# Performance work log

Measured on AMD Instinct MI355X. Metric: run time of the kernel, lower is better.

## Reference

```python
import jax, jax.numpy as jnp
import numpy as np

NUM_CODES = 8192
DIM = 512
COMMITMENT_COST = 0.25


def setup_inputs() -> dict:
    key = jax.random.key(0)
    kx, kc = jax.random.split(key)
    x = jax.random.normal(kx, (8, 4096, DIM), dtype=jnp.float32)
    # nn.init.uniform_(codebook.weight, -1/num_codes, 1/num_codes)
    bound = 1.0 / NUM_CODES
    codebook = jax.random.uniform(kc, (NUM_CODES, DIM), dtype=jnp.float32,
                                  minval=-bound, maxval=bound)
    return {"x": x, "codebook": codebook}


def reference(x, codebook):
    orig_shape = x.shape
    flat = x.reshape(-1, orig_shape[-1])              # [N, D]
    # Squared-distance expansion (argmin-equivalent to torch.cdist's L2):
    # ||f||^2 - 2 f.c + ||c||^2
    x_sq = jnp.sum(flat * flat, axis=-1, keepdims=True)          # [N, 1]
    c_sq = jnp.sum(codebook * codebook, axis=-1)                 # [K]
    dists = x_sq - 2.0 * jnp.einsum('nd,kd->nk', flat, codebook) + c_sq  # [N, K]
    indices_flat = jnp.argmin(dists, axis=-1)                    # [N] int
    quantized_flat = codebook[indices_flat]                      # [N, D]
    # codebook_loss = mse(quantized, sg(flat)); commitment = mse(flat, sg(quantized))
    codebook_loss = jnp.mean((quantized_flat - jax.lax.stop_gradient(flat)) ** 2)
    commitment_loss = jnp.mean((flat - jax.lax.stop_gradient(quantized_flat)) ** 2)
    vq_loss = codebook_loss + COMMITMENT_COST * commitment_loss
    # straight-through
    quantized_st = flat + jax.lax.stop_gradient(quantized_flat - flat)
    return (quantized_st.reshape(orig_shape), vq_loss,
            indices_flat.reshape(orig_shape[:-1]))
```

## Files before the change

### kernel.cpp

```cpp
#include <hip/hip_runtime.h>


#define NROWS 32768
#define KCODES 8192
#define DD 512
#define CAP 24
#define MARGIN 2.5e-4f

typedef __bf16 bf16_t;
typedef __bf16 bf16x4 __attribute__((ext_vector_type(4)));
typedef __bf16 bf16x8 __attribute__((ext_vector_type(8)));
typedef float f32x4 __attribute__((ext_vector_type(4)));

__device__ __forceinline__ int lofs(int row, int s) {
  return row * 32 + (((s ^ ((row >> 1) & 3))) << 3);
}

__device__ __forceinline__ void gld16(const bf16_t* g, bf16_t* l) {
  __builtin_amdgcn_global_load_lds(
      (const __attribute__((address_space(1))) void*)g,
      (__attribute__((address_space(3))) void*)l, 16, 0, 0);
}

__global__ __launch_bounds__(256) void prep_kernel(const float* __restrict__ in,
                                                   float* __restrict__ out_sq,
                                                   bf16_t* __restrict__ outb,
                                                   int nrows) {
  const int wave = threadIdx.x >> 6;
  const int lane = threadIdx.x & 63;
  const int row = blockIdx.x * 4 + wave;
  if (row >= nrows) return;
  const float* p = in + (size_t)row * DD;
  double s = 0.0;
#pragma unroll
  for (int j = 0; j < DD / 64; ++j) {
    float v = p[j * 64 + lane];
    float sq = v * v;
    s += (double)sq;
  }
  for (int off = 32; off > 0; off >>= 1) s += __shfl_down(s, off, 64);
  if (lane == 0) out_sq[row] = (float)s;
  const float4* p4 = (const float4*)p;
  float4 a = p4[lane * 2];
  float4 b = p4[lane * 2 + 1];
  bf16x8 o = {(bf16_t)a.x, (bf16_t)a.y, (bf16_t)a.z, (bf16_t)a.w,
              (bf16_t)b.x, (bf16_t)b.y, (bf16_t)b.z, (bf16_t)b.w};
  *(bf16x8*)(outb + (size_t)row * DD + lane * 8) = o;
}

__global__ __launch_bounds__(256, 2) void coarse_kernel(
    const bf16_t* __restrict__ xbf, const bf16_t* __restrict__ cbbf,
    const float* __restrict__ csq, int* __restrict__ cnt_g,
    int* __restrict__ list_g) {
  __shared__ bf16_t As[128 * 32];
  __shared__ bf16_t Bs[128 * 32];
  __shared__ unsigned best[128];
  __shared__ int cnt_l[128];
  __shared__ int list_l[128 * CAP];

  const int tid = threadIdx.x;
  const int w = tid >> 6;
  const int lane = tid & 63;
  const int q = lane >> 4;
  const int l15 = lane & 15;
  const int rOff = (w & 1) * 64;
  const int cOff = (w >> 1) * 64;

  const int bid = blockIdx.x;
  const int xcd = bid & 7;
  const int g = bid >> 3;
  const int half = xcd >> 2;
  const int rowblk = (xcd & 3) * 64 + g;
  const int row0 = rowblk * 128;
  const int cbase = half * (KCODES / 2);

  for (int i = tid; i < 128; i += 256) { best[i] = 0xFFFFFFFFu; cnt_l[i] = 0; }

  const int sub = lane >> 2;
  const int pos = lane & 3;
  const bf16_t *agp[2], *bgp[2];
  bf16_t *alp[2], *blp[2];
#pragma unroll
  for (int a = 0; a < 2; ++a) {
    const int row = w * 32 + a * 16 + sub;
    const int sg = pos ^ ((row >> 1) & 3);
    agp[a] = xbf + (size_t)(row0 + row) * DD + sg * 8;
    alp[a] = As + row * 32 + pos * 8;
    bgp[a] = cbbf + (size_t)(cbase + row) * DD + sg * 8;
    blp[a] = Bs + row * 32 + pos * 8;
  }

  int afofs[4], bfofs[4];
#pragma unroll
  for (int rt = 0; rt < 4; ++rt) afofs[rt] = lofs(rOff + rt * 16 + l15, q);
#pragma unroll
  for (int ct = 0; ct < 4; ++ct) bfofs[ct] = lofs(cOff + ct * 16 + l15, q);

  __syncthreads();

#pragma unroll 1
  for (int ci = 0; ci < (KCODES / 2) / 128; ++ci) {
    const int c0 = cbase + ci * 128;
    const size_t coff = (size_t)(ci * 128) * DD;
    f32x4 acc[4][4];
#pragma unroll
    for (int rt = 0; rt < 4; ++rt)
#pragma unroll
      for (int ct = 0; ct < 4; ++ct) {
        f32x4 z = {0.f, 0.f, 0.f, 0.f};
        acc[rt][ct] = z;
      }

#pragma unroll 1
    for (int kc = 0; kc < DD / 32; ++kc) {
      const int kb = kc * 32;
      __syncthreads();
      gld16(agp[0] + kb, alp[0]);
      gld16(agp[1] + kb, alp[1]);
      gld16(bgp[0] + coff + kb, blp[0]);
      gld16(bgp[1] + coff + kb, blp[1]);
      __syncthreads();

      bf16x8 af[4], bfr[4];
#pragma unroll
      for (int rt = 0; rt < 4; ++rt) af[rt] = *(const bf16x8*)&As[afofs[rt]];
#pragma unroll
      for (int ct = 0; ct < 4; ++ct) bfr[ct] = *(const bf16x8*)&Bs[bfofs[ct]];
#pragma unroll
      for (int rt = 0; rt < 4; ++rt)
#pragma unroll
        for (int ct = 0; ct < 4; ++ct)
          acc[rt][ct] = __builtin_amdgcn_mfma_f32_16x16x32_bf16(
              af[rt], bfr[ct], acc[rt][ct], 0, 0, 0);
    }

    float cs1[4];
#pragma unroll
    for (int ct = 0; ct < 4; ++ct)
      cs1[ct] = 1.0f + csq[c0 + cOff + ct * 16 + l15];

#pragma unroll
    for (int rt = 0; rt < 4; ++rt) {
#pragma unroll
      for (int reg = 0; reg < 4; ++reg) {
        float m = fmaf(-2.0f, acc[rt][0][reg], cs1[0]);
#pragma unroll
        for (int ct = 1; ct < 4; ++ct) {
          float d = fmaf(-2.0f, acc[rt][ct][reg], cs1[ct]);
          m = fminf(m, d);
        }
        unsigned mb = __float_as_uint(m);
#pragma unroll
        for (int msk = 1; msk <= 8; msk <<= 1) {
          unsigned o = __shfl_xor(mb, msk, 64);
          mb = mb < o ? mb : o;
        }
        if (l15 == 0) atomicMin(&best[rOff + rt * 16 + q * 4 + reg], mb);
      }
    }
    __syncthreads();

#pragma unroll
    for (int rt = 0; rt < 4; ++rt) {
#pragma unroll
      for (int reg = 0; reg < 4; ++reg) {
        const int rloc = rOff + rt * 16 + q * 4 + reg;
        const float thr = __uint_as_float(best[rloc]) + MARGIN;
#pragma unroll
        for (int ct = 0; ct < 4; ++ct) {
          float d = fmaf(-2.0f, acc[rt][ct][reg], cs1[ct]);
          if (d <= thr) {
            int pos2 = atomicAdd(&cnt_l[rloc], 1);
            if (pos2 < CAP)
              list_l[rloc * CAP + pos2] = c0 + cOff + ct * 16 + l15;
          }
        }
      }
    }
    __syncthreads();
  }

  for (int i = tid; i < 128; i += 256) cnt_g[(row0 + i) * 2 + half] = cnt_l[i];
  for (int i = tid; i < 128 * CAP; i += 256) {
    const int r = i / CAP, p = i % CAP;
    list_g[((size_t)(row0 + r) * 2 + half) * CAP + p] = list_l[i];
  }
}

__global__ __launch_bounds__(256) void rescore_kernel(
    const float* __restrict__ x, const float* __restrict__ cb,
    const float* __restrict__ xsq, const float* __restrict__ csq,
    const int* __restrict__ list, const int* __restrict__ cnt,
    int* __restrict__ idxbuf) {
  const int row = blockIdx.x * 4 + (threadIdx.x >> 6);
  const int lane = threadIdx.x & 63;
  const int n0 = cnt[row * 2];
  const int n1 = cnt[row * 2 + 1];
  const float xs = xsq[row];
  const float4* xr4 = (const float4*)(x + (size_t)row * DD);
  unsigned long long bestv = ~0ULL;

  if (n0 >= 1 && n0 <= CAP && n1 >= 0 && n1 <= CAP && (n0 + n1) <= 56) {
    int myidx = -1;
    if (lane < n0) myidx = list[((size_t)row * 2) * CAP + lane];
    else if (lane - n0 < n1) myidx = list[((size_t)row * 2 + 1) * CAP + (lane - n0)];
    if (myidx >= 0) {
      const float4* cr4 = (const float4*)(cb + (size_t)myidx * DD);
      float acc = 0.0f;
      for (int k4 = 0; k4 < DD / 4; ++k4) {
        float4 xv = xr4[k4];
        float4 cv = cr4[k4];
        acc = fmaf(xv.x, cv.x, acc);
        acc = fmaf(xv.y, cv.y, acc);
        acc = fmaf(xv.z, cv.z, acc);
        acc = fmaf(xv.w, cv.w, acc);
      }
      float t = xs - 2.0f * acc;
      float d = t + csq[myidx];
      bestv = ((unsigned long long)__float_as_uint(d) << 32) | (unsigned)myidx;
    }
  } else {
    for (int idx = lane; idx < KCODES; idx += 64) {
      const float4* cr4 = (const float4*)(cb + (size_t)idx * DD);
      float acc = 0.0f;
      for (int k4 = 0; k4 < DD / 4; ++k4) {
        float4 xv = xr4[k4];
        float4 cv = cr4[k4];
        acc = fmaf(xv.x, cv.x, acc);
        acc = fmaf(xv.y, cv.y, acc);
        acc = fmaf(xv.z, cv.z, acc);
        acc = fmaf(xv.w, cv.w, acc);
      }
      float t = xs - 2.0f * acc;
      float d = t + csq[idx];
      unsigned long long pk =
          ((unsigned long long)__float_as_uint(d) << 32) | (unsigned)idx;
      if (pk < bestv) bestv = pk;
    }
  }
#pragma unroll
  for (int s = 1; s <= 32; s <<= 1) {
    unsigned long long o = __shfl_xor(bestv, s, 64);
    if (o < bestv) bestv = o;
  }
  if (lane == 0) idxbuf[row] = (int)(bestv & 0xffffffffu);
}

__global__ __launch_bounds__(128) void epilogue_kernel(
    const float* __restrict__ x, const float* __restrict__ cb,
    const int* __restrict__ idxbuf, float* __restrict__ out_q,
    float* __restrict__ out_idx_f, double* __restrict__ partials) {
  const int row = blockIdx.x;
  const int t = threadIdx.x;
  const int k = idxbuf[row];

  const float4* xr = (const float4*)(x + (size_t)row * DD);
  const float4* qr = (const float4*)(cb + (size_t)k * DD);
  float4* orow = (float4*)(out_q + (size_t)row * DD);

  float4 xv = xr[t];
  float4 qv = qr[t];
  float dx = qv.x - xv.x, dy = qv.y - xv.y, dz = qv.z - xv.z, dw = qv.w - xv.w;
  float4 o;
  o.x = xv.x + dx; o.y = xv.y + dy; o.z = xv.z + dz; o.w = xv.w + dw;
  orow[t] = o;

  float s0 = dx * dx, s1 = dy * dy, s2 = dz * dz, s3 = dw * dw;
  double part = (double)s0 + (double)s1 + (double)s2 + (double)s3;
  for (int off = 32; off > 0; off >>= 1) part += __shfl_down(part, off, 64);
  __shared__ double red[2];
  const int lane = t & 63, wv = t >> 6;
  if (lane == 0) red[wv] = part;
  __syncthreads();
  if (t == 0) {
    partials[row] = red[0] + red[1];
    out_idx_f[row] = (float)k;
  }
}

__global__ __launch_bounds__(256) void finalize_kernel(
    const double* __restrict__ partials, float* __restrict__ out_loss) {
  __shared__ double red[256];
  double s = 0.0;
  for (int i = threadIdx.x; i < NROWS; i += 256) s += partials[i];
  red[threadIdx.x] = s;
  __syncthreads();
  for (int st = 128; st > 0; st >>= 1) {
    if (threadIdx.x < st) red[threadIdx.x] += red[threadIdx.x + st];
    __syncthreads();
  }
  if (threadIdx.x == 0) {
    double mean = red[0] / ((double)NROWS * (double)DD);
    float cl = (float)mean;
    out_loss[0] = cl + 0.25f * cl;
  }
}

extern "C" void kernel_launch(void* const* d_in, const int* in_sizes, int n_in,
                              void* d_out, int out_size, void* d_ws,
                              size_t ws_size, hipStream_t stream) {
  const float* x = (const float*)d_in[0];
  const float* cb = (const float*)d_in[1];
  float* out = (float*)d_out;

  char* ws = (char*)d_ws;
  double* partials = (double*)ws;
  int* idxbuf = (int*)(ws + 262144);
  float* csq = (float*)(ws + 262144 + 131072);
  float* xsq = (float*)(ws + 262144 + 131072 + 32768);
  int* cnt = (int*)(ws + 262144 + 131072 + 32768 + 131072);
  int* list = (int*)(ws + 262144 + 131072 + 32768 + 131072 + 262144);

  bf16_t* cbbf = (bf16_t*)d_out;
  bf16_t* xbf = cbbf + (size_t)KCODES * DD;

  prep_kernel<<<KCODES / 4, 256, 0, stream>>>(cb, csq, cbbf, KCODES);
  prep_kernel<<<NROWS / 4, 256, 0, stream>>>(x, xsq, xbf, NROWS);
  coarse_kernel<<<512, 256, 0, stream>>>(xbf, cbbf, csq, cnt, list);
  rescore_kernel<<<NROWS / 4, 256, 0, stream>>>(x, cb, xsq, csq, list, cnt, idxbuf);
  epilogue_kernel<<<NROWS, 128, 0, stream>>>(x, cb, idxbuf, out,
                                             out + 16777216 + 1, partials);
  finalize_kernel<<<1, 256, 0, stream>>>(partials, out + 16777216);
}
```

Measured before the change: 948.1 us.

## Double-buffer coarse GEMM, split codebook in quarters, fuse rescore with epilogue

Result: slower. 2.521 ms (+165.9%).

```diff
diff --git a/kernel.cpp b/kernel.cpp
--- a/kernel.cpp
+++ b/kernel.cpp
@@ -4,11 +4,10 @@
 #define NROWS 32768
 #define KCODES 8192
 #define DD 512
-#define CAP 24
+#define CAP 12
 #define MARGIN 2.5e-4f
 
 typedef __bf16 bf16_t;
-typedef __bf16 bf16x4 __attribute__((ext_vector_type(4)));
 typedef __bf16 bf16x8 __attribute__((ext_vector_type(8)));
 typedef float f32x4 __attribute__((ext_vector_type(4)));
 
@@ -48,12 +47,12 @@
   *(bf16x8*)(outb + (size_t)row * DD + lane * 8) = o;
 }
 
-__global__ __launch_bounds__(256, 2) void coarse_kernel(
+__global__ __launch_bounds__(256, 3) void coarse_kernel(
     const bf16_t* __restrict__ xbf, const bf16_t* __restrict__ cbbf,
-    const float* __restrict__ csq, int* __restrict__ cnt_g,
+    const float* __restrict__ csq, unsigned char* __restrict__ cnt_g,
     int* __restrict__ list_g) {
-  __shared__ bf16_t As[128 * 32];
-  __shared__ bf16_t Bs[128 * 32];
+  __shared__ bf16_t As[2][128 * 32];
+  __shared__ bf16_t Bs[2][128 * 32];
   __shared__ unsigned best[128];
   __shared__ int cnt_l[128];
   __shared__ int list_l[128 * CAP];
@@ -69,25 +68,27 @@
   const int bid = blockIdx.x;
   const int xcd = bid & 7;
   const int g = bid >> 3;
-  const int half = xcd >> 2;
-  const int rowblk = (xcd & 3) * 64 + g;
+  const int qtr = xcd >> 1;
+  const int rowblk = (xcd & 1) * 128 + g;
   const int row0 = rowblk * 128;
-  const int cbase = half * (KCODES / 2);
+  const int cbase = qtr * (KCODES / 4);
+  const int NCI = (KCODES / 4) / 128;
+  const int NSTEP = NCI * (DD / 32);
 
   for (int i = tid; i < 128; i += 256) { best[i] = 0xFFFFFFFFu; cnt_l[i] = 0; }
 
   const int sub = lane >> 2;
   const int pos = lane & 3;
   const bf16_t *agp[2], *bgp[2];
-  bf16_t *alp[2], *blp[2];
+  int aofs[2], bofs[2];
 #pragma unroll
   for (int a = 0; a < 2; ++a) {
     const int row = w * 32 + a * 16 + sub;
     const int sg = pos ^ ((row >> 1) & 3);
     agp[a] = xbf + (size_t)(row0 + row) * DD + sg * 8;
-    alp[a] = As + row * 32 + pos * 8;
+    aofs[a] = row * 32 + pos * 8;
     bgp[a] = cbbf + (size_t)(cbase + row) * DD + sg * 8;
-    blp[a] = Bs + row * 32 + pos * 8;
+    bofs[a] = row * 32 + pos * 8;
   }
 
   int afofs[4], bfofs[4];
@@ -96,13 +97,43 @@
 #pragma unroll
   for (int ct = 0; ct < 4; ++ct) bfofs[ct] = lofs(cOff + ct * 16 + l15, q);
 
+  gld16(agp[0], &As[0][aofs[0]]);
+  gld16(agp[1], &As[0][aofs[1]]);
+  gld16(bgp[0], &Bs[0][bofs[0]]);
+  gld16(bgp[1], &Bs[0][bofs[1]]);
   __syncthreads();
 
+  f32x4 acc[4][4];
+
+#define PIPE_STEP(S, CUR)                                                     \
+  do {                                                                        \
+    const int sN = (S) + 1;                                                   \
+    if (sN < NSTEP) {                                                         \
+      const int kbN = (sN & (DD / 32 - 1)) * 32;                              \
+      const size_t coffN = (size_t)((sN >> 4) * 128) * DD;                    \
+      gld16(agp[0] + kbN, &As[(CUR) ^ 1][aofs[0]]);                           \
+      gld16(agp[1] + kbN, &As[(CUR) ^ 1][aofs[1]]);                           \
+      gld16(bgp[0] + coffN + kbN, &Bs[(CUR) ^ 1][bofs[0]]);                   \
+      gld16(bgp[1] + coffN + kbN, &Bs[(CUR) ^ 1][bofs[1]]);                   \
+    }                                                                         \
+    bf16x8 af[4], bfr[4];                                                     \
+    _Pragma("unroll") for (int rt = 0; rt < 4; ++rt)                          \
+        af[rt] = *(const bf16x8*)&As[(CUR)][afofs[rt]];                       \
+    _Pragma("unroll") for (int ct = 0; ct < 4; ++ct)                          \
+        bfr[ct] = *(const bf16x8*)&Bs[(CUR)][bfofs[ct]];                      \
+    _Pragma("unroll") for (int rt = 0; rt < 4; ++rt)                          \
+        _Pragma("unroll") for (int ct = 0; ct < 4; ++ct)                      \
+            acc[rt][ct] = __builtin_amdgcn_mfma_f32_16x16x32_bf16(            \
+                af[rt], bfr[ct], acc[rt][ct], 0, 0, 0);                       \
+    asm volatile("s_waitcnt vmcnt(0)" ::: "memory");                          \
+    __builtin_amdgcn_sched_barrier(0);                                        \
+    __builtin_amdgcn_s_barrier();                                             \
+    __builtin_amdgcn_sched_barrier(0);                                        \
+  } while (0)
+
 #pragma unroll 1
-  for (int ci = 0; ci < (KCODES / 2) / 128; ++ci) {
+  for (int ci = 0; ci < NCI; ++ci) {
     const int c0 = cbase + ci * 128;
-    const size_t coff = (size_t)(ci * 128) * DD;
-    f32x4 acc[4][4];
 #pragma unroll
     for (int rt = 0; rt < 4; ++rt)
 #pragma unroll
@@ -112,26 +143,10 @@
       }
 
 #pragma unroll 1
-    for (int kc = 0; kc < DD / 32; ++kc) {
-      const int kb = kc * 32;
-      __syncthreads();
-      gld16(agp[0] + kb, alp[0]);
-      gld16(agp[1] + kb, alp[1]);
-      gld16(bgp[0] + coff + kb, blp[0]);
-      gld16(bgp[1] + coff + kb, blp[1]);
-      __syncthreads();
-
-      bf16x8 af[4], bfr[4];
-#pragma unroll
-      for (int rt = 0; rt < 4; ++rt) af[rt] = *(const bf16x8*)&As[afofs[rt]];
-#pragma unroll
-      for (int ct = 0; ct < 4; ++ct) bfr[ct] = *(const bf16x8*)&Bs[bfofs[ct]];
-#pragma unroll
-      for (int rt = 0; rt < 4; ++rt)
-#pragma unroll
-        for (int ct = 0; ct < 4; ++ct)
-          acc[rt][ct] = __builtin_amdgcn_mfma_f32_16x16x32_bf16(
-              af[rt], bfr[ct], acc[rt][ct], 0, 0, 0);
+    for (int kc2 = 0; kc2 < (DD / 32) / 2; ++kc2) {
+      const int s = ci * (DD / 32) + kc2 * 2;
+      PIPE_STEP(s, 0);
+      PIPE_STEP(s + 1, 1);
     }
 
     float cs1[4];
@@ -179,31 +194,43 @@
     }
     __syncthreads();
   }
-
-  for (int i = tid; i < 128; i += 256) cnt_g[(row0 + i) * 2 + half] = cnt_l[i];
+#undef PIPE_STEP
+
+  for (int i = tid; i < 128; i += 256) {
+    int c = cnt_l[i];
+    cnt_g[(size_t)(row0 + i) * 4 + qtr] = (unsigned char)(c > CAP ? CAP + 1 : c);
+  }
   for (int i = tid; i < 128 * CAP; i += 256) {
     const int r = i / CAP, p = i % CAP;
-    list_g[((size_t)(row0 + r) * 2 + half) * CAP + p] = list_l[i];
-  }
-}
-
-__global__ __launch_bounds__(256) void rescore_kernel(
+    list_g[((size_t)(row0 + r) * 4 + qtr) * CAP + p] = list_l[i];
+  }
+}
+
+__global__ __launch_bounds__(256) void rescore_epilogue_kernel(
     const float* __restrict__ x, const float* __restrict__ cb,
     const float* __restrict__ xsq, const float* __restrict__ csq,
-    const int* __restrict__ list, const int* __restrict__ cnt,
-    int* __restrict__ idxbuf) {
+    const int* __restrict__ list, const unsigned char* __restrict__ cnt,
+    float* __restrict__ out_q, float* __restrict__ out_idx_f,
+    double* __restrict__ partials) {
   const int row = blockIdx.x * 4 + (threadIdx.x >> 6);
   const int lane = threadIdx.x & 63;
-  const int n0 = cnt[row * 2];
-  const int n1 = cnt[row * 2 + 1];
+  const unsigned char* c4 = cnt + (size_t)row * 4;
+  const int n0 = c4[0], n1 = c4[1], n2 = c4[2], n3 = c4[3];
+  const int t0 = n0, t1 = t0 + n1, t2 = t1 + n2, t3 = t2 + n3;
   const float xs = xsq[row];
   const float4* xr4 = (const float4*)(x + (size_t)row * DD);
   unsigned long long bestv = ~0ULL;
 
-  if (n0 >= 1 && n0 <= CAP && n1 >= 0 && n1 <= CAP && (n0 + n1) <= 56) {
+  if (n0 <= CAP && n1 <= CAP && n2 <= CAP && n3 <= CAP && t3 >= 1) {
     int myidx = -1;
-    if (lane < n0) myidx = list[((size_t)row * 2) * CAP + lane];
-    else if (lane - n0 < n1) myidx = list[((size_t)row * 2 + 1) * CAP + (lane - n0)];
+    if (lane < t3) {
+      int seg, off;
+      if (lane < t0)      { seg = 0; off = lane; }
+      else if (lane < t1) { seg = 1; off = lane - t0; }
+      else if (lane < t2) { seg = 2; off = lane - t1; }
+      else                { seg = 3; off = lane - t2; }
+      myidx = list[((size_t)row * 4 + seg) * CAP + off];
+    }
     if (myidx >= 0) {
       const float4* cr4 = (const float4*)(cb + (size_t)myidx * DD);
       float acc = 0.0f;
@@ -243,37 +270,31 @@
     unsigned long long o = __shfl_xor(bestv, s, 64);
     if (o < bestv) bestv = o;
   }
-  if (lane == 0) idxbuf[row] = (int)(bestv & 0xffffffffu);
-}
-
-__global__ __launch_bounds__(128) void epilogue_kernel(
-    const float* __restrict__ x, const float* __restrict__ cb,
-    const int* __restrict__ idxbuf, float* __restrict__ out_q,
-    float* __restrict__ out_idx_f, double* __restrict__ partials) {
-  const int row = blockIdx.x;
-  const int t = threadIdx.x;
-  const int k = idxbuf[row];
-
-  const float4* xr = (const float4*)(x + (size_t)row * DD);
+  const int k = (int)(bestv & 0xffffffffu);
+
   const float4* qr = (const float4*)(cb + (size_t)k * DD);
   float4* orow = (float4*)(out_q + (size_t)row * DD);
 
-  float4 xv = xr[t];
-  float4 qv = qr[t];
-  float dx = qv.x - xv.x, dy = qv.y - xv.y, dz = qv.z - xv.z, dw = qv.w - xv.w;
-  float4 o;
-  o.x = xv.x + dx; o.y = xv.y + dy; o.z = xv.z + dz; o.w = xv.w + dw;
-  orow[t] = o;
-
-  float s0 = dx * dx, s1 = dy * dy, s2 = dz * dz, s3 = dw * dw;
-  double part = (double)s0 + (double)s1 + (double)s2 + (double)s3;
-  for (int off = 32; off > 0; off >>= 1) part += __shfl_down(part, off, 64);
-  __shared__ double red[2];
-  const int lane = t & 63, wv = t >> 6;
-  if (lane == 0) red[wv] = part;
-  __syncthreads();
-  if (t == 0) {
-    partials[row] = red[0] + red[1];
+  float4 xa = xr4[lane], qa = qr[lane];
+  float dax = qa.x - xa.x, day = qa.y - xa.y, daz = qa.z - xa.z, daw = qa.w - xa.w;
+  float4 oa;
+  oa.x = xa.x + dax; oa.y = xa.y + day; oa.z = xa.z + daz; oa.w = xa.w + daw;
+  orow[lane] = oa;
+  double pa = (double)(dax * dax) + (double)(day * day) +
+              (double)(daz * daz) + (double)(daw * daw);
+
+  float4 xb = xr4[lane + 64], qb = qr[lane + 64];
+  float dbx = qb.x - xb.x, dby = qb.y - xb.y, dbz = qb.z - xb.z, dbw = qb.w - xb.w;
+  float4 ob;
+  ob.x = xb.x + dbx; ob.y = xb.y + dby; ob.z = xb.z + dbz; ob.w = xb.w + dbw;
+  orow[lane + 64] = ob;
+  double pb = (double)(dbx * dbx) + (double)(dby * dby) +
+              (double)(dbz * dbz) + (double)(dbw * dbw);
+
+  for (int off = 32; off > 0; off >>= 1) pa += __shfl_down(pa, off, 64);
+  for (int off = 32; off > 0; off >>= 1) pb += __shfl_down(pb, off, 64);
+  if (lane == 0) {
+    partials[row] = pa + pb;
     out_idx_f[row] = (float)k;
   }
 }
@@ -305,20 +326,18 @@
 
   char* ws = (char*)d_ws;
   double* partials = (double*)ws;
-  int* idxbuf = (int*)(ws + 262144);
-  float* csq = (float*)(ws + 262144 + 131072);
-  float* xsq = (float*)(ws + 262144 + 131072 + 32768);
-  int* cnt = (int*)(ws + 262144 + 131072 + 32768 + 131072);
-  int* list = (int*)(ws + 262144 + 131072 + 32768 + 131072 + 262144);
+  float* csq = (float*)(ws + 262144);
+  float* xsq = (float*)(ws + 262144 + 32768);
+  unsigned char* cnt = (unsigned char*)(ws + 262144 + 32768 + 131072);
+  int* list = (int*)(ws + 262144 + 32768 + 131072 + 131072);
 
   bf16_t* cbbf = (bf16_t*)d_out;
   bf16_t* xbf = cbbf + (size_t)KCODES * DD;
 
   prep_kernel<<<KCODES / 4, 256, 0, stream>>>(cb, csq, cbbf, KCODES);
   prep_kernel<<<NROWS / 4, 256, 0, stream>>>(x, xsq, xbf, NROWS);
-  coarse_kernel<<<512, 256, 0, stream>>>(xbf, cbbf, csq, cnt, list);
-  rescore_kernel<<<NROWS / 4, 256, 0, stream>>>(x, cb, xsq, csq, list, cnt, idxbuf);
-  epilogue_kernel<<<NROWS, 128, 0, stream>>>(x, cb, idxbuf, out,
-                                             out + 16777216 + 1, partials);
+  coarse_kernel<<<1024, 256, 0, stream>>>(xbf, cbbf, csq, cnt, list);
+  rescore_epilogue_kernel<<<NROWS / 4, 256, 0, stream>>>(
+      x, cb, xsq, csq, list, cnt, out, out + 16777216 + 1, partials);
   finalize_kernel<<<1, 256, 0, stream>>>(partials, out + 16777216);
 }
```
